# Optimization experiments

Hardware: AMD Instinct MI355X
Metric: run time of the kernel (lower is better)

## Reference

```python
import jax, jax.numpy as jnp
import numpy as np

N_NODES, N_EDGES = 50000, 800000
NODE_DIM, EDGE_DIM, HIDDEN, HEADS = 128, 64, 128, 8
HEAD_DIM = HIDDEN // HEADS


def setup_inputs() -> dict:
    key = jax.random.key(0)
    ks = jax.random.split(key, 24)

    def lin(k, fan_in, fan_out):
        lim = 1.0 / np.sqrt(fan_in)
        kw, kb = jax.random.split(k)
        W = jax.random.uniform(kw, (fan_in, fan_out), jnp.float32, -lim, lim)
        b = jax.random.uniform(kb, (fan_out,), jnp.float32, -lim, lim)
        return W, b

    inp = {}
    inp["nodes"] = jax.random.normal(ks[0], (N_NODES, NODE_DIM), jnp.float32)
    inp["edges"] = jax.random.normal(ks[1], (N_EDGES, EDGE_DIM), jnp.float32)
    inp["edge_index"] = jax.random.randint(ks[2], (2, N_EDGES), 0, N_NODES, jnp.int32)
    inp["conservation_scores"] = jax.random.uniform(ks[3], (N_NODES, 1), jnp.float32)
    inp["distances"] = jax.random.uniform(ks[4], (N_EDGES, 1), jnp.float32)

    inp["Wq"], inp["bq"] = lin(ks[5], NODE_DIM, HIDDEN)
    inp["Wk"], inp["bk"] = lin(ks[6], NODE_DIM, HIDDEN)
    inp["Wv"], inp["bv"] = lin(ks[7], NODE_DIM, HIDDEN)
    inp["We"], inp["be"] = lin(ks[8], EDGE_DIM, HEADS)
    inp["Wc1"], inp["bc1"] = lin(ks[9], 1, 32)
    inp["Wc2"], inp["bc2"] = lin(ks[10], 32, HEADS)
    inp["Wd1"], inp["bd1"] = lin(ks[11], 1, 16)
    inp["Wd2"], inp["bd2"] = lin(ks[12], 16, HEADS)
    inp["Wo"], inp["bo"] = lin(ks[13], HIDDEN, NODE_DIM)
    inp["gamma"] = jnp.ones((NODE_DIM,), jnp.float32)
    inp["beta"] = jnp.zeros((NODE_DIM,), jnp.float32)
    return inp


def reference(nodes, edges, edge_index, conservation_scores, distances,
              Wq, bq, Wk, bk, Wv, bv, We, be,
              Wc1, bc1, Wc2, bc2, Wd1, bd1, Wd2, bd2,
              Wo, bo, gamma, beta):
    N = nodes.shape[0]
    src, tgt = edge_index[0], edge_index[1]

    q = (nodes @ Wq + bq).reshape(N, HEADS, HEAD_DIM)
    k = (nodes @ Wk + bk).reshape(N, HEADS, HEAD_DIM)
    v = (nodes @ Wv + bv).reshape(N, HEADS, HEAD_DIM)

    # per-edge attention scores [E, H]
    scores = jnp.einsum("ehd,ehd->eh", q[src], k[tgt]) / np.sqrt(HEAD_DIM)
    scores = scores + edges @ We + be

    # conservation bias (sigmoid MLP), gathered at target nodes, multiplicative
    cons = jax.nn.sigmoid(jax.nn.relu(conservation_scores @ Wc1 + bc1) @ Wc2 + bc2)
    scores = scores * cons[tgt]

    # distance bias (MLP on edge distances), additive
    scores = scores + jax.nn.relu(distances @ Wd1 + bd1) @ Wd2 + bd2

    # segment softmax over incoming edges of each target node
    seg_max = jax.ops.segment_max(scores, tgt, num_segments=N)  # [N, H]
    w = jnp.exp(scores - seg_max[tgt])
    seg_sum = jax.ops.segment_sum(w, tgt, num_segments=N)  # [N, H]
    weights = w / seg_sum[tgt]

    # weighted scatter-add aggregation
    attended = weights[..., None] * v[tgt]  # [E, H, D]
    agg = jax.ops.segment_sum(attended, tgt, num_segments=N).reshape(N, HIDDEN)

    out = agg @ Wo + bo
    x = nodes + out  # dropout is identity in eval mode
    mu = jnp.mean(x, axis=-1, keepdims=True)
    var = jnp.var(x, axis=-1, keepdims=True)
    return (x - mu) / jnp.sqrt(var + 1e-5) * gamma + beta
```

## Files before the change

### kernel.cpp

```cpp
#include <hip/hip_runtime.h>

#define NN 50000
#define NE 800000
#define D  128
#define TR 32



__global__ __launch_bounds__(256) void prep_kernel(
    const float* __restrict__ Wv, const float* __restrict__ bv,
    const float* __restrict__ Wo,
    float* __restrict__ Wc, float* __restrict__ bc, int* __restrict__ mask)
{
    int b = blockIdx.x, t = threadIdx.x;
    if (b < 64) {
        int k = 2 * b + (t >> 7);
        int j = t & 127;
        float acc = 0.f;
        #pragma unroll 4
        for (int m = 0; m < 128; ++m)
            acc = fmaf(Wv[k * 128 + m], Wo[m * 128 + j], acc);
        Wc[k * 128 + j] = acc;
    } else if (b == 64) {
        if (t < 128) {
            float acc = 0.f;
            #pragma unroll 4
            for (int m = 0; m < 128; ++m)
                acc = fmaf(bv[m], Wo[m * 128 + t], acc);
            bc[t] = acc;
        }
    } else {
        int i = (b - 65) * 256 + t;
        if (i < NN) mask[i] = 0;
    }
}

__global__ __launch_bounds__(256) void scatter_kernel(
    const int* __restrict__ tgt, int* __restrict__ mask)
{
    int e = blockIdx.x * 256 + threadIdx.x;
    if (e < NE) mask[tgt[e]] = 1;
}

__global__ __launch_bounds__(256, 3) void fused_kernel(
    const float* __restrict__ nodes,
    const float* __restrict__ Wc, const float* __restrict__ bc,
    const int* __restrict__ mask,
    const float* __restrict__ bo,
    const float* __restrict__ gamma, const float* __restrict__ beta,
    float* __restrict__ out)
{
    __shared__ float Wl[64 * 128];
    __shared__ float Ndl[TR * 128];
    __shared__ int   Ml[TR];

    const int tid  = threadIdx.x;
    const int cg   = tid & 31;
    const int slot = tid >> 5;
    const int rbase = slot * 4;

    const float4 bo4 = ((const float4*)bo)[cg];
    const float4 bc4 = ((const float4*)bc)[cg];
    const float4 g4  = ((const float4*)gamma)[cg];
    const float4 be4 = ((const float4*)beta)[cg];

    const int ntiles = (NN + TR - 1) / TR;
    for (int tile = blockIdx.x; tile < ntiles; tile += gridDim.x) {
        const int r0 = tile * TR;
        __syncthreads();

        #pragma unroll
        for (int i = 0; i < 4; ++i) {
            int f  = tid + 256 * i;
            int rr = f >> 5, cc = f & 31;
            int gr = r0 + rr;
            float4 v = make_float4(0.f, 0.f, 0.f, 0.f);
            if (gr < NN) v = ((const float4*)nodes)[gr * 32 + cc];
            ((float4*)Ndl)[f] = v;
        }
        if (tid < TR) {
            int gr = r0 + tid;
            Ml[tid] = (gr < NN) ? mask[gr] : 0;
        }

        float4 acc[4];
        acc[0] = acc[1] = acc[2] = acc[3] = make_float4(0.f, 0.f, 0.f, 0.f);

        #pragma unroll
        for (int h = 0; h < 2; ++h) {
            if (h) __syncthreads();
            const float4* Wsrc = (const float4*)(Wc + h * 64 * 128);
            #pragma unroll
            for (int i = 0; i < 8; ++i)
                ((float4*)Wl)[tid + 256 * i] = Wsrc[tid + 256 * i];
            __syncthreads();

            #pragma unroll 2
            for (int k4 = 0; k4 < 16; ++k4) {
                const float4* wr = (const float4*)(Wl + k4 * 4 * 128);
                float4 w0 = wr[cg];
                float4 w1 = wr[32 + cg];
                float4 w2 = wr[64 + cg];
                float4 w3 = wr[96 + cg];
                #pragma unroll
                for (int rr = 0; rr < 4; ++rr) {
                    float4 nv = ((const float4*)(Ndl + (rbase + rr) * 128))[h * 16 + k4];
                    acc[rr].x = fmaf(nv.x, w0.x, acc[rr].x);
                    acc[rr].x = fmaf(nv.y, w1.x, acc[rr].x);
                    acc[rr].x = fmaf(nv.z, w2.x, acc[rr].x);
                    acc[rr].x = fmaf(nv.w, w3.x, acc[rr].x);
                    acc[rr].y = fmaf(nv.x, w0.y, acc[rr].y);
                    acc[rr].y = fmaf(nv.y, w1.y, acc[rr].y);
                    acc[rr].y = fmaf(nv.z, w2.y, acc[rr].y);
                    acc[rr].y = fmaf(nv.w, w3.y, acc[rr].y);
                    acc[rr].z = fmaf(nv.x, w0.z, acc[rr].z);
                    acc[rr].z = fmaf(nv.y, w1.z, acc[rr].z);
                    acc[rr].z = fmaf(nv.z, w2.z, acc[rr].z);
                    acc[rr].z = fmaf(nv.w, w3.z, acc[rr].z);
                    acc[rr].w = fmaf(nv.x, w0.w, acc[rr].w);
                    acc[rr].w = fmaf(nv.y, w1.w, acc[rr].w);
                    acc[rr].w = fmaf(nv.z, w2.w, acc[rr].w);
                    acc[rr].w = fmaf(nv.w, w3.w, acc[rr].w);
                }
            }
        }

        #pragma unroll
        for (int rr = 0; rr < 4; ++rr) {
            int r = r0 + rbase + rr;
            float4 nd = ((const float4*)(Ndl + (rbase + rr) * 128))[cg];
            float m = (Ml[rbase + rr] != 0) ? 1.f : 0.f;
            float4 x;
            x.x = nd.x + bo4.x + m * (acc[rr].x + bc4.x);
            x.y = nd.y + bo4.y + m * (acc[rr].y + bc4.y);
            x.z = nd.z + bo4.z + m * (acc[rr].z + bc4.z);
            x.w = nd.w + bo4.w + m * (acc[rr].w + bc4.w);

            float s  = x.x + x.y + x.z + x.w;
            float ss = x.x * x.x + x.y * x.y + x.z * x.z + x.w * x.w;
            #pragma unroll
            for (int off = 1; off < 32; off <<= 1) {
                s  += __shfl_xor(s, off);
                ss += __shfl_xor(ss, off);
            }
            float mu   = s * (1.f / 128.f);
            float var  = ss * (1.f / 128.f) - mu * mu;
            float rstd = rsqrtf(var + 1e-5f);

            float4 o;
            o.x = (x.x - mu) * rstd * g4.x + be4.x;
            o.y = (x.y - mu) * rstd * g4.y + be4.y;
            o.z = (x.z - mu) * rstd * g4.z + be4.z;
            o.w = (x.w - mu) * rstd * g4.w + be4.w;
            if (r < NN) ((float4*)out)[r * 32 + cg] = o;
        }
    }
}

extern "C" void kernel_launch(void* const* d_in, const int* in_sizes, int n_in,
                              void* d_out, int out_size, void* d_ws, size_t ws_size,
                              hipStream_t stream) {
    const float* nodes = (const float*)d_in[0];
    const int*   ei    = (const int*)d_in[2];
    const float* Wv    = (const float*)d_in[9];
    const float* bv    = (const float*)d_in[10];
    const float* Wo    = (const float*)d_in[21];
    const float* bo    = (const float*)d_in[22];
    const float* gamma = (const float*)d_in[23];
    const float* beta  = (const float*)d_in[24];

    float* Wc   = (float*)d_ws;
    float* bc   = Wc + 16384;
    int*   mask = (int*)(bc + 128);

    prep_kernel<<<65 + (NN + 255) / 256, 256, 0, stream>>>(Wv, bv, Wo, Wc, bc, mask);
    scatter_kernel<<<(NE + 255) / 256, 256, 0, stream>>>(ei + NE, mask);
    fused_kernel<<<768, 256, 0, stream>>>(nodes, Wc, bc, mask, bo, gamma, beta,
                                          (float*)d_out);
}
```

Measured before the change: 343.4 us.

## Use 64-row tiles with async LDS loads and fold scatter into prep kernel

The fused kernel now handles one 64-row tile per block with 8 rows per thread instead of looping over 32-row tiles. Node rows and weights are loaded into LDS with global_load_lds async copies, and the mask bits are read into registers. The mask scatter moves into the weight-prep kernel using int4 reads, and mask zeroing becomes its own small vectorized kernel. The intent is higher arithmetic intensity and less launch and loop overhead, at the cost of more registers and lower occupancy (launch bounds drop from 3 to 2).

```diff
diff --git a/kernel.cpp b/kernel.cpp
--- a/kernel.cpp
+++ b/kernel.cpp
@@ -2,14 +2,25 @@
 
 #define NN 50000
 #define NE 800000
-#define D  128
-#define TR 32
+#define TRF 64
 
 
+__device__ __forceinline__ void async_copy16(void* lds_dst, const void* gsrc) {
+    __builtin_amdgcn_global_load_lds(
+        (const __attribute__((address_space(1))) void*)gsrc,
+        (__attribute__((address_space(3))) void*)lds_dst,
+        16, 0, 0);
+}
 
-__global__ __launch_bounds__(256) void prep_kernel(
+__global__ __launch_bounds__(256) void init_mask_kernel(int* __restrict__ mask)
+{
+    int i = blockIdx.x * 256 + threadIdx.x;
+    if (i < NN / 4) ((int4*)mask)[i] = make_int4(0, 0, 0, 0);
+}
+
+__global__ __launch_bounds__(256) void prep_scatter_kernel(
     const float* __restrict__ Wv, const float* __restrict__ bv,
-    const float* __restrict__ Wo,
+    const float* __restrict__ Wo, const int* __restrict__ tgt,
     float* __restrict__ Wc, float* __restrict__ bc, int* __restrict__ mask)
 {
     int b = blockIdx.x, t = threadIdx.x;
@@ -31,18 +42,14 @@
         }
     } else {
         int i = (b - 65) * 256 + t;
-        if (i < NN) mask[i] = 0;
+        if (i < NE / 4) {
+            int4 e = ((const int4*)tgt)[i];
+            mask[e.x] = 1; mask[e.y] = 1; mask[e.z] = 1; mask[e.w] = 1;
+        }
     }
 }
 
-__global__ __launch_bounds__(256) void scatter_kernel(
-    const int* __restrict__ tgt, int* __restrict__ mask)
-{
-    int e = blockIdx.x * 256 + threadIdx.x;
-    if (e < NE) mask[tgt[e]] = 1;
-}
-
-__global__ __launch_bounds__(256, 3) void fused_kernel(
+__global__ __launch_bounds__(256, 2) void fused_kernel(
     const float* __restrict__ nodes,
     const float* __restrict__ Wc, const float* __restrict__ bc,
     const int* __restrict__ mask,
@@ -51,109 +58,113 @@
     float* __restrict__ out)
 {
     __shared__ float Wl[64 * 128];
-    __shared__ float Ndl[TR * 128];
-    __shared__ int   Ml[TR];
+    __shared__ float Ndl[TRF * 128];
 
-    const int tid  = threadIdx.x;
-    const int cg   = tid & 31;
-    const int slot = tid >> 5;
-    const int rbase = slot * 4;
+    const int tid   = threadIdx.x;
+    const int cg    = tid & 31;
+    const int slot  = tid >> 5;
+    const int rbase = slot * 8;
+    const int r0    = blockIdx.x * TRF;
+
+    #pragma unroll
+    for (int i = 0; i < 8; ++i) {
+        int f  = tid + 256 * i;
+        int gr = r0 + (f >> 5);
+        if (gr > NN - 1) gr = NN - 1;
+        async_copy16((float4*)Ndl + f, (const float4*)nodes + gr * 32 + (f & 31));
+    }
+    #pragma unroll
+    for (int i = 0; i < 8; ++i) {
+        int f = tid + 256 * i;
+        async_copy16((float4*)Wl + f, (const float4*)Wc + f);
+    }
+    int mbits = 0;
+    #pragma unroll
+    for (int rr = 0; rr < 8; ++rr) {
+        int r = r0 + rbase + rr;
+        if (r < NN && mask[r]) mbits |= (1 << rr);
+    }
 
     const float4 bo4 = ((const float4*)bo)[cg];
     const float4 bc4 = ((const float4*)bc)[cg];
     const float4 g4  = ((const float4*)gamma)[cg];
     const float4 be4 = ((const float4*)beta)[cg];
 
-    const int ntiles = (NN + TR - 1) / TR;
-    for (int tile = blockIdx.x; tile < ntiles; tile += gridDim.x) {
-        const int r0 = tile * TR;
-        __syncthreads();
+    float4 acc[8];
+    #pragma unroll
+    for (int rr = 0; rr < 8; ++rr) acc[rr] = make_float4(0.f, 0.f, 0.f, 0.f);
 
-        #pragma unroll
-        for (int i = 0; i < 4; ++i) {
-            int f  = tid + 256 * i;
-            int rr = f >> 5, cc = f & 31;
-            int gr = r0 + rr;
-            float4 v = make_float4(0.f, 0.f, 0.f, 0.f);
-            if (gr < NN) v = ((const float4*)nodes)[gr * 32 + cc];
-            ((float4*)Ndl)[f] = v;
+    __syncthreads();
+
+    #pragma unroll
+    for (int h = 0; h < 2; ++h) {
+        if (h) {
+            __syncthreads();
+            #pragma unroll
+            for (int i = 0; i < 8; ++i) {
+                int f = tid + 256 * i;
+                async_copy16((float4*)Wl + f, (const float4*)(Wc + 64 * 128) + f);
+            }
+            __syncthreads();
         }
-        if (tid < TR) {
-            int gr = r0 + tid;
-            Ml[tid] = (gr < NN) ? mask[gr] : 0;
-        }
-
-        float4 acc[4];
-        acc[0] = acc[1] = acc[2] = acc[3] = make_float4(0.f, 0.f, 0.f, 0.f);
-
-        #pragma unroll
-        for (int h = 0; h < 2; ++h) {
-            if (h) __syncthreads();
-            const float4* Wsrc = (const float4*)(Wc + h * 64 * 128);
+        #pragma unroll 2
+        for (int k4 = 0; k4 < 16; ++k4) {
+            const float4* wr = (const float4*)(Wl + k4 * 4 * 128);
+            float4 w0 = wr[cg];
+            float4 w1 = wr[32 + cg];
+            float4 w2 = wr[64 + cg];
+            float4 w3 = wr[96 + cg];
             #pragma unroll
-            for (int i = 0; i < 8; ++i)
-                ((float4*)Wl)[tid + 256 * i] = Wsrc[tid + 256 * i];
-            __syncthreads();
-
-            #pragma unroll 2
-            for (int k4 = 0; k4 < 16; ++k4) {
-                const float4* wr = (const float4*)(Wl + k4 * 4 * 128);
-                float4 w0 = wr[cg];
-                float4 w1 = wr[32 + cg];
-                float4 w2 = wr[64 + cg];
-                float4 w3 = wr[96 + cg];
-                #pragma unroll
-                for (int rr = 0; rr < 4; ++rr) {
-                    float4 nv = ((const float4*)(Ndl + (rbase + rr) * 128))[h * 16 + k4];
-                    acc[rr].x = fmaf(nv.x, w0.x, acc[rr].x);
-                    acc[rr].x = fmaf(nv.y, w1.x, acc[rr].x);
-                    acc[rr].x = fmaf(nv.z, w2.x, acc[rr].x);
-                    acc[rr].x = fmaf(nv.w, w3.x, acc[rr].x);
-                    acc[rr].y = fmaf(nv.x, w0.y, acc[rr].y);
-                    acc[rr].y = fmaf(nv.y, w1.y, acc[rr].y);
-                    acc[rr].y = fmaf(nv.z, w2.y, acc[rr].y);
-                    acc[rr].y = fmaf(nv.w, w3.y, acc[rr].y);
-                    acc[rr].z = fmaf(nv.x, w0.z, acc[rr].z);
-                    acc[rr].z = fmaf(nv.y, w1.z, acc[rr].z);
-                    acc[rr].z = fmaf(nv.z, w2.z, acc[rr].z);
-                    acc[rr].z = fmaf(nv.w, w3.z, acc[rr].z);
-                    acc[rr].w = fmaf(nv.x, w0.w, acc[rr].w);
-                    acc[rr].w = fmaf(nv.y, w1.w, acc[rr].w);
-                    acc[rr].w = fmaf(nv.z, w2.w, acc[rr].w);
-                    acc[rr].w = fmaf(nv.w, w3.w, acc[rr].w);
-                }
+            for (int rr = 0; rr < 8; ++rr) {
+                float4 nv = ((const float4*)(Ndl + (rbase + rr) * 128))[h * 16 + k4];
+                acc[rr].x = fmaf(nv.x, w0.x, acc[rr].x);
+                acc[rr].x = fmaf(nv.y, w1.x, acc[rr].x);
+                acc[rr].x = fmaf(nv.z, w2.x, acc[rr].x);
+                acc[rr].x = fmaf(nv.w, w3.x, acc[rr].x);
+                acc[rr].y = fmaf(nv.x, w0.y, acc[rr].y);
+                acc[rr].y = fmaf(nv.y, w1.y, acc[rr].y);
+                acc[rr].y = fmaf(nv.z, w2.y, acc[rr].y);
+                acc[rr].y = fmaf(nv.w, w3.y, acc[rr].y);
+                acc[rr].z = fmaf(nv.x, w0.z, acc[rr].z);
+                acc[rr].z = fmaf(nv.y, w1.z, acc[rr].z);
+                acc[rr].z = fmaf(nv.z, w2.z, acc[rr].z);
+                acc[rr].z = fmaf(nv.w, w3.z, acc[rr].z);
+                acc[rr].w = fmaf(nv.x, w0.w, acc[rr].w);
+                acc[rr].w = fmaf(nv.y, w1.w, acc[rr].w);
+                acc[rr].w = fmaf(nv.z, w2.w, acc[rr].w);
+                acc[rr].w = fmaf(nv.w, w3.w, acc[rr].w);
             }
         }
+    }
 
+    #pragma unroll
+    for (int rr = 0; rr < 8; ++rr) {
+        int r = r0 + rbase + rr;
+        float4 nd = ((const float4*)(Ndl + (rbase + rr) * 128))[cg];
+        float m = ((mbits >> rr) & 1) ? 1.f : 0.f;
+        float4 x;
+        x.x = nd.x + bo4.x + m * (acc[rr].x + bc4.x);
+        x.y = nd.y + bo4.y + m * (acc[rr].y + bc4.y);
+        x.z = nd.z + bo4.z + m * (acc[rr].z + bc4.z);
+        x.w = nd.w + bo4.w + m * (acc[rr].w + bc4.w);
+
+        float s  = x.x + x.y + x.z + x.w;
+        float ss = x.x * x.x + x.y * x.y + x.z * x.z + x.w * x.w;
         #pragma unroll
-        for (int rr = 0; rr < 4; ++rr) {
-            int r = r0 + rbase + rr;
-            float4 nd = ((const float4*)(Ndl + (rbase + rr) * 128))[cg];
-            float m = (Ml[rbase + rr] != 0) ? 1.f : 0.f;
-            float4 x;
-            x.x = nd.x + bo4.x + m * (acc[rr].x + bc4.x);
-            x.y = nd.y + bo4.y + m * (acc[rr].y + bc4.y);
-            x.z = nd.z + bo4.z + m * (acc[rr].z + bc4.z);
-            x.w = nd.w + bo4.w + m * (acc[rr].w + bc4.w);
+        for (int off = 1; off < 32; off <<= 1) {
+            s  += __shfl_xor(s, off);
+            ss += __shfl_xor(ss, off);
+        }
+        float mu   = s * (1.f / 128.f);
+        float var  = ss * (1.f / 128.f) - mu * mu;
+        float rstd = rsqrtf(var + 1e-5f);
 
-            float s  = x.x + x.y + x.z + x.w;
-            float ss = x.x * x.x + x.y * x.y + x.z * x.z + x.w * x.w;
-            #pragma unroll
-            for (int off = 1; off < 32; off <<= 1) {
-                s  += __shfl_xor(s, off);
-                ss += __shfl_xor(ss, off);
-            }
-            float mu   = s * (1.f / 128.f);
-            float var  = ss * (1.f / 128.f) - mu * mu;
-            float rstd = rsqrtf(var + 1e-5f);
-
-            float4 o;
-            o.x = (x.x - mu) * rstd * g4.x + be4.x;
-            o.y = (x.y - mu) * rstd * g4.y + be4.y;
-            o.z = (x.z - mu) * rstd * g4.z + be4.z;
-            o.w = (x.w - mu) * rstd * g4.w + be4.w;
-            if (r < NN) ((float4*)out)[r * 32 + cg] = o;
-        }
+        float4 o;
+        o.x = (x.x - mu) * rstd * g4.x + be4.x;
+        o.y = (x.y - mu) * rstd * g4.y + be4.y;
+        o.z = (x.z - mu) * rstd * g4.z + be4.z;
+        o.w = (x.w - mu) * rstd * g4.w + be4.w;
+        if (r < NN) ((float4*)out)[r * 32 + cg] = o;
     }
 }
 
@@ -173,8 +184,9 @@
     float* bc   = Wc + 16384;
     int*   mask = (int*)(bc + 128);
 
-    prep_kernel<<<65 + (NN + 255) / 256, 256, 0, stream>>>(Wv, bv, Wo, Wc, bc, mask);
-    scatter_kernel<<<(NE + 255) / 256, 256, 0, stream>>>(ei + NE, mask);
-    fused_kernel<<<768, 256, 0, stream>>>(nodes, Wc, bc, mask, bo, gamma, beta,
-                                          (float*)d_out);
+    init_mask_kernel<<<(NN / 4 + 255) / 256, 256, 0, stream>>>(mask);
+    prep_scatter_kernel<<<65 + (NE / 4 + 255) / 256, 256, 0, stream>>>(
+        Wv, bv, Wo, ei + NE, Wc, bc, mask);
+    fused_kernel<<<(NN + TRF - 1) / TRF, 256, 0, stream>>>(
+        nodes, Wc, bc, mask, bo, gamma, beta, (float*)d_out);
 }
```

New measurement: 344.4 us. Within noise of the previous version (+0.3%).
